# Optimization experiments

Hardware: AMD Instinct MI355X
Metric: run time of the kernel (lower is better)

Reference implementation:

```python
import jax, jax.numpy as jnp
import numpy as np

N = 100000
E = 1600000
F_IN = 32
H = 64
EDGE_DIM = 2
OUT = 1
NEG_SLOPE = 0.2


def setup_inputs() -> dict:
    key = jax.random.key(0)
    ks = jax.random.split(key, 20)
    g = lambda k, shape, fan_in: jax.random.normal(k, shape, jnp.float32) / np.sqrt(fan_in)
    inp = {
        "x": jax.random.normal(ks[0], (N, F_IN), jnp.float32),
        "edge_index": jax.random.randint(ks[1], (2, E), 0, N, jnp.int32),
        "edge_attr": jax.random.normal(ks[2], (E, EDGE_DIM), jnp.float32),
        # GATConv layer 1 (in=F_IN, out=H, heads=1, edge_dim=EDGE_DIM)
        "W1": g(ks[3], (F_IN, H), F_IN),
        "as1": g(ks[4], (H,), H),
        "ad1": g(ks[5], (H,), H),
        "We1": g(ks[6], (EDGE_DIM, H), EDGE_DIM),
        "ae1": g(ks[7], (H,), H),
        "b1": jnp.zeros((H,), jnp.float32),
        # GATConv layer 2 (in=H, out=H)
        "W2": g(ks[8], (H, H), H),
        "as2": g(ks[9], (H,), H),
        "ad2": g(ks[10], (H,), H),
        "We2": g(ks[11], (EDGE_DIM, H), EDGE_DIM),
        "ae2": g(ks[12], (H,), H),
        "b2": jnp.zeros((H,), jnp.float32),
        # Linear head
        "Wl": g(ks[13], (H, OUT), H),
        "bl": jnp.zeros((OUT,), jnp.float32),
    }
    return inp


def gat_conv(x, src, dst, edge_attr, W, att_src, att_dst, We, att_e, bias):
    """PyG GATConv, heads=1, add_self_loops=True (fill_value='mean'), eval mode."""
    n = x.shape[0]
    # add self-loops; self-loop edge_attr = mean of edge_attr (fill_value='mean')
    loop_attr = jnp.mean(edge_attr, axis=0)
    src_a = jnp.concatenate([src, jnp.arange(n, dtype=src.dtype)])
    dst_a = jnp.concatenate([dst, jnp.arange(n, dtype=dst.dtype)])
    ea = jnp.concatenate([edge_attr, jnp.broadcast_to(loop_attr, (n, edge_attr.shape[1]))])
    h = x @ W                          # [n, H]
    a_src = h @ att_src                # [n]
    a_dst = h @ att_dst                # [n]
    a_edge = (ea @ We) @ att_e         # [E+n]
    alpha = a_src[src_a] + a_dst[dst_a] + a_edge
    alpha = jax.nn.leaky_relu(alpha, NEG_SLOPE)
    # segment softmax over incoming edges of each destination node
    amax = jax.ops.segment_max(alpha, dst_a, num_segments=n)
    ex = jnp.exp(alpha - amax[dst_a])
    denom = jax.ops.segment_sum(ex, dst_a, num_segments=n)
    w = ex / denom[dst_a]              # every node has a self-loop -> denom > 0
    out = jax.ops.segment_sum(h[src_a] * w[:, None], dst_a, num_segments=n)
    return out + bias


def reference(x, edge_index, edge_attr, W1, as1, ad1, We1, ae1, b1,
              W2, as2, ad2, We2, ae2, b2, Wl, bl):
    src, dst = edge_index[0], edge_index[1]
    h = gat_conv(x, src, dst, edge_attr, W1, as1, ad1, We1, ae1, b1)
    h = jax.nn.relu(h)  # dropout is identity in eval mode
    h = gat_conv(h, src, dst, edge_attr, W2, as2, ad2, We2, ae2, b2)
    h = h @ Wl + bl
    return jax.nn.relu(h)
```

## Files before the change

### kernel.cpp

```cpp
#include <hip/hip_runtime.h>
#include <hip/hip_fp16.h>
#include <cstdint>

#define HH 64
#define NEG 0.2f
#define NB 256
#define SH 7
#define BKCAP 1024
#define ECAP 4096
#define CHCAP 6272

__device__ __forceinline__ float leaky(float x){ return x > 0.f ? x : NEG * x; }

__global__ void k_hist(const int* __restrict__ dst, const float* __restrict__ ea,
                       int* __restrict__ ghist, float2* __restrict__ pbuf,
                       int E, int nbkt, int CH){
    __shared__ int hist[BKCAP];
    __shared__ float2 sm[8];
    for (int i = threadIdx.x; i < nbkt; i += 512) hist[i] = 0;
    __syncthreads();
    int b = blockIdx.x;
    int e0 = b * CH, e1 = min(E, e0 + CH);
    float s0 = 0.f, s1 = 0.f;
    for (int e = e0 + threadIdx.x; e < e1; e += 512){
        int d = dst[e];
        atomicAdd(&hist[d >> SH], 1);
        float2 v = *reinterpret_cast<const float2*>(ea + 2ll * e);
        s0 += v.x; s1 += v.y;
    }
    #pragma unroll
    for (int o = 32; o; o >>= 1){ s0 += __shfl_xor(s0, o); s1 += __shfl_xor(s1, o); }
    int wv = threadIdx.x >> 6;
    if ((threadIdx.x & 63) == 0) sm[wv] = make_float2(s0, s1);
    __syncthreads();
    if (threadIdx.x == 0){
        float m0 = 0.f, m1 = 0.f;
        #pragma unroll
        for (int i = 0; i < 8; ++i){ m0 += sm[i].x; m1 += sm[i].y; }
        pbuf[b] = make_float2(m0, m1);
    }
    for (int i = threadIdx.x; i < nbkt; i += 512)
        ghist[(size_t)b * nbkt + i] = hist[i];
}

__global__ void k_const(const float* __restrict__ We1, const float* __restrict__ ae1,
                        const float* __restrict__ We2, const float* __restrict__ ae2,
                        const float2* __restrict__ pbuf, float* __restrict__ cbuf,
                        float invE, int nbp){
    int k = threadIdx.x;
    float m0 = 0.f, m1 = 0.f;
    for (int i = k; i < nbp; i += 64){ float2 u = pbuf[i]; m0 += u.x; m1 += u.y; }
    float p0 = We1[k] * ae1[k], p1 = We1[64 + k] * ae1[k];
    float q0 = We2[k] * ae2[k], q1 = We2[64 + k] * ae2[k];
    #pragma unroll
    for (int o = 32; o; o >>= 1){
        m0 += __shfl_xor(m0, o); m1 += __shfl_xor(m1, o);
        p0 += __shfl_xor(p0, o); p1 += __shfl_xor(p1, o);
        q0 += __shfl_xor(q0, o); q1 += __shfl_xor(q1, o);
    }
    if (k == 0){
        m0 *= invE; m1 *= invE;
        cbuf[4] = p0; cbuf[5] = p1; cbuf[6] = q0; cbuf[7] = q1;
        cbuf[2] = m0 * p0 + m1 * p1;
        cbuf[3] = m0 * q0 + m1 * q1;
    }
}

__global__ void k_scanA(const int* __restrict__ ghist, int* __restrict__ incl,
                        int* __restrict__ part, int M, int nbkt){
    __shared__ int sm[256];
    int tid = threadIdx.x;
    int i = blockIdx.x * 256 + tid;
    int v = 0;
    if (i < M) v = ghist[(size_t)(i % NB) * nbkt + (i / NB)];
    int x = v;
    sm[tid] = x; __syncthreads();
    for (int o = 1; o < 256; o <<= 1){
        int t = (tid >= o) ? sm[tid - o] : 0;
        __syncthreads();
        x += t; sm[tid] = x;
        __syncthreads();
    }
    if (i < M) incl[i] = x;
    if (tid == 255) part[blockIdx.x] = x;
}

__global__ void k_scanB(int* __restrict__ part, int nb){
    __shared__ int sm[1024];
    int tid = threadIdx.x;
    int C = (nb + 1023) >> 10;
    if (C > 8) C = 8;
    int base = tid * C;
    int vals[8];
    int s = 0;
    #pragma unroll
    for (int k = 0; k < 8; ++k){
        if (k < C){
            int i = base + k;
            int v = (i < nb) ? part[i] : 0;
            vals[k] = v; s += v;
        }
    }
    sm[tid] = s; __syncthreads();
    int x = s;
    for (int o = 1; o < 1024; o <<= 1){
        int t = (tid >= o) ? sm[tid - o] : 0;
        __syncthreads();
        x += t; sm[tid] = x;
        __syncthreads();
    }
    int excl = x - s;
    #pragma unroll
    for (int k = 0; k < 8; ++k){
        if (k < C){
            int i = base + k;
            if (i < nb){ int v = vals[k]; part[i] = excl; excl += v; }
        }
    }
}

__global__ void k_scanC(const int* __restrict__ ghist, const int* __restrict__ incl,
                        const int* __restrict__ part, int* __restrict__ gbase,
                        int M, int nbkt){
    int i = blockIdx.x * 256 + threadIdx.x;
    if (i < M){
        int v = ghist[(size_t)(i % NB) * nbkt + (i / NB)];
        gbase[i] = part[blockIdx.x] + incl[i] - v;
    }
}

__global__ void k_scatter2(const int* __restrict__ src, const int* __restrict__ dst,
                           const float* __restrict__ ea, const int* __restrict__ ghist,
                           const int* __restrict__ gbase, const float* __restrict__ cbuf,
                           uint2* __restrict__ csort, int E, int nbkt, int CH){
    __shared__ uint2 srec[CHCAP];
    __shared__ unsigned short bktof[CHCAP];
    __shared__ int gb[BKCAP];
    __shared__ int cur[BKCAP];
    __shared__ int wsum[512];
    int tid = threadIdx.x;
    int b = blockIdx.x;
    int base2 = tid * 2;
    int v0 = 0, v1 = 0;
    if (base2 < nbkt)     v0 = ghist[(size_t)b * nbkt + base2];
    if (base2 + 1 < nbkt) v1 = ghist[(size_t)b * nbkt + base2 + 1];
    int s = v0 + v1;
    wsum[tid] = s; __syncthreads();
    int x = s;
    for (int o = 1; o < 512; o <<= 1){
        int t = (tid >= o) ? wsum[tid - o] : 0;
        __syncthreads();
        x += t; wsum[tid] = x;
        __syncthreads();
    }
    int excl = x - s;
    if (base2 < nbkt)     cur[base2]     = excl;
    if (base2 + 1 < nbkt) cur[base2 + 1] = excl + v0;
    __syncthreads();
    for (int i = tid; i < nbkt; i += 512)
        gb[i] = gbase[(size_t)i * NB + b] - cur[i];
    __syncthreads();
    float c4 = cbuf[4], c5 = cbuf[5], c6 = cbuf[6], c7 = cbuf[7];
    int e0 = b * CH, e1 = min(E, e0 + CH);
    for (int e = e0 + tid; e < e1; e += 512){
        int d = dst[e];
        int bkt = d >> SH;
        float2 v = *reinterpret_cast<const float2*>(ea + 2ll * e);
        float a1 = v.x * c4 + v.y * c5;
        float a2 = v.x * c6 + v.y * c7;
        __half2 ah = __floats2half2_rn(a1, a2);
        int p = atomicAdd(&cur[bkt], 1);
        uint2 o;
        o.x = (unsigned)src[e] | ((unsigned)(d & ((1 << SH) - 1)) << 20);
        o.y = *reinterpret_cast<unsigned*>(&ah);
        srec[p] = o;
        bktof[p] = (unsigned short)bkt;
    }
    __syncthreads();
    int cnt = e1 - e0;
    for (int j = tid; j < cnt; j += 512)
        csort[gb[bktof[j]] + j] = srec[j];
}

__global__ void __launch_bounds__(256, 1) k_bucket(
        const uint2* __restrict__ csort, const int* __restrict__ gbase,
        uint2* __restrict__ rec, int* __restrict__ row_ptr,
        int E, int n, int nbkt){
    __shared__ uint2 lrec[ECAP];
    __shared__ uint2 srec[ECAP];
    __shared__ int nhist[128], ncur[128], sscan[128];
    int tid = threadIdx.x;
    int bkt = blockIdx.x;
    int base = gbase[(size_t)bkt * NB];
    int end  = (bkt + 1 < nbkt) ? gbase[(size_t)(bkt + 1) * NB] : E;
    int cnt = min(end - base, ECAP);
    if (tid < 128) nhist[tid] = 0;
    __syncthreads();
    for (int j = tid; j < cnt; j += 256){
        uint2 r = csort[base + j];
        lrec[j] = r;
        atomicAdd(&nhist[(r.x >> 20) & 127], 1);
    }
    __syncthreads();
    int v = (tid < 128) ? nhist[tid] : 0;
    if (tid < 128) sscan[tid] = v;
    __syncthreads();
    for (int o = 1; o < 128; o <<= 1){
        int t = 0;
        if (tid < 128 && tid >= o) t = sscan[tid - o];
        __syncthreads();
        if (tid < 128) sscan[tid] += t;
        __syncthreads();
    }
    if (tid < 128){
        int st = sscan[tid] - v;
        ncur[tid] = st;
        int node = (bkt << SH) + tid;
        if (node < n) row_ptr[node] = base + st;
    }
    if (bkt == 0 && tid == 255) row_ptr[n] = E;
    __syncthreads();
    for (int j = tid; j < cnt; j += 256){
        uint2 r = lrec[j];
        int dl = (r.x >> 20) & 127;
        int p = atomicAdd(&ncur[dl], 1);
        srec[p] = make_uint2(r.x & 0xFFFFFu, r.y);
    }
    __syncthreads();
    for (int j = tid; j < cnt; j += 256)
        rec[base + j] = srec[j];
}

template<int F, bool HALFIN>
__global__ void k_feat(const void* __restrict__ inp, const float* __restrict__ W,
                       const float* __restrict__ as_, const float* __restrict__ ad_,
                       __half* __restrict__ h, float* __restrict__ asrc,
                       float* __restrict__ adst, int n){
    int lane = threadIdx.x & 63;
    int wid0 = (blockIdx.x * blockDim.x + threadIdx.x) >> 6;
    int nw   = (gridDim.x * blockDim.x) >> 6;
    float wcol[F];
    #pragma unroll
    for (int i = 0; i < F; ++i) wcol[i] = W[i * HH + lane];
    float asl = as_[lane], adl = ad_[lane];
    for (int wid = wid0; wid < n; wid += nw){
        int u = __builtin_amdgcn_readfirstlane(wid);
        float a0 = 0.f, a1 = 0.f, a2 = 0.f, a3 = 0.f;
        if constexpr (!HALFIN){
            const float* __restrict__ row = (const float*)inp + (size_t)u * F;
            #pragma unroll
            for (int i = 0; i < F; i += 4){
                a0 += row[i]     * wcol[i];
                a1 += row[i + 1] * wcol[i + 1];
                a2 += row[i + 2] * wcol[i + 2];
                a3 += row[i + 3] * wcol[i + 3];
            }
        } else {
            const unsigned* __restrict__ row =
                (const unsigned*)((const __half*)inp + (size_t)u * F);
            #pragma unroll
            for (int i = 0; i < F / 2; i += 2){
                unsigned p0 = row[i], p1 = row[i + 1];
                __half2 h0 = *reinterpret_cast<__half2*>(&p0);
                __half2 h1 = *reinterpret_cast<__half2*>(&p1);
                float2 f0 = __half22float2(h0), f1 = __half22float2(h1);
                a0 += f0.x * wcol[2 * i];
                a1 += f0.y * wcol[2 * i + 1];
                a2 += f1.x * wcol[2 * i + 2];
                a3 += f1.y * wcol[2 * i + 3];
            }
        }
        float acc = (a0 + a1) + (a2 + a3);
        h[(size_t)u * HH + lane] = __float2half(acc);
        float vs = acc * asl, vd = acc * adl;
        #pragma unroll
        for (int o = 32; o; o >>= 1){ vs += __shfl_xor(vs, o); vd += __shfl_xor(vd, o); }
        if (lane == 0){ asrc[u] = vs; adst[u] = vd; }
    }
}

template<int AFIELD, bool RELU, bool HEAD>
__global__ void k_fused(const __half* __restrict__ h, const uint2* __restrict__ rec,
                        const int* __restrict__ row_ptr, const float* __restrict__ asrc,
                        const float* __restrict__ adst, const float* __restrict__ cbuf,
                        const float* __restrict__ bias, const float* __restrict__ Wl,
                        const float* __restrict__ bl, __half* __restrict__ outh,
                        float* __restrict__ outf, int n){
    int tid  = blockIdx.x * blockDim.x + threadIdx.x;
    int wave = tid >> 6;
    int lane = threadIdx.x & 63;
    int grp  = lane >> 3;
    int l7   = lane & 7;
    int node = wave * 8 + grp;
    bool valid = node < n;
    int nc = valid ? node : 0;
    int b  = row_ptr[nc];
    int e2 = valid ? row_ptr[nc + 1] : b;
    float ad = adst[nc];
    float aself = leaky(asrc[nc] + ad + cbuf[AFIELD == 1 ? 2 : 3]);
    float exs = __expf(aself);
    float dsum = exs;
    float acc[8];
    {
        float4 q = *reinterpret_cast<const float4*>(h + (size_t)nc * HH + (l7 << 3));
        const __half2* ph = reinterpret_cast<const __half2*>(&q);
        #pragma unroll
        for (int i = 0; i < 4; ++i){
            float2 f = __half22float2(ph[i]);
            acc[2 * i]     = exs * f.x;
            acc[2 * i + 1] = exs * f.y;
        }
    }
    auto pick = [](uint2 rr) -> float {
        __half2 ah = *reinterpret_cast<const __half2*>(&rr.y);
        return (AFIELD == 1) ? __low2float(ah) : __high2float(ah);
    };
    int j = b;
    for (; j + 3 < e2; j += 4){
        uint2 r0 = rec[j], r1 = rec[j + 1], r2 = rec[j + 2], r3 = rec[j + 3];
        int s0 = (int)r0.x, s1 = (int)r1.x, s2 = (int)r2.x, s3 = (int)r3.x;
        float w0 = __expf(leaky(asrc[s0] + ad + pick(r0)));
        float w1 = __expf(leaky(asrc[s1] + ad + pick(r1)));
        float w2 = __expf(leaky(asrc[s2] + ad + pick(r2)));
        float w3 = __expf(leaky(asrc[s3] + ad + pick(r3)));
        dsum += (w0 + w1) + (w2 + w3);
        float4 q0 = *reinterpret_cast<const float4*>(h + (size_t)s0 * HH + (l7 << 3));
        float4 q1 = *reinterpret_cast<const float4*>(h + (size_t)s1 * HH + (l7 << 3));
        float4 q2 = *reinterpret_cast<const float4*>(h + (size_t)s2 * HH + (l7 << 3));
        float4 q3 = *reinterpret_cast<const float4*>(h + (size_t)s3 * HH + (l7 << 3));
        const __half2* p0 = reinterpret_cast<const __half2*>(&q0);
        const __half2* p1 = reinterpret_cast<const __half2*>(&q1);
        const __half2* p2 = reinterpret_cast<const __half2*>(&q2);
        const __half2* p3 = reinterpret_cast<const __half2*>(&q3);
        #pragma unroll
        for (int i = 0; i < 4; ++i){
            float2 f0 = __half22float2(p0[i]);
            float2 f1 = __half22float2(p1[i]);
            float2 f2 = __half22float2(p2[i]);
            float2 f3 = __half22float2(p3[i]);
            acc[2 * i]     += w0 * f0.x + w1 * f1.x + w2 * f2.x + w3 * f3.x;
            acc[2 * i + 1] += w0 * f0.y + w1 * f1.y + w2 * f2.y + w3 * f3.y;
        }
    }
    for (; j < e2; ++j){
        uint2 rr = rec[j];
        int s = (int)rr.x;
        float w = __expf(leaky(asrc[s] + ad + pick(rr)));
        dsum += w;
        float4 q = *reinterpret_cast<const float4*>(h + (size_t)s * HH + (l7 << 3));
        const __half2* ph = reinterpret_cast<const __half2*>(&q);
        #pragma unroll
        for (int i = 0; i < 4; ++i){
            float2 f = __half22float2(ph[i]);
            acc[2 * i]     += w * f.x;
            acc[2 * i + 1] += w * f.y;
        }
    }
    float inv = 1.f / dsum;
    float4 b0 = *reinterpret_cast<const float4*>(bias + (l7 << 3));
    float4 b1 = *reinterpret_cast<const float4*>(bias + (l7 << 3) + 4);
    float r[8];
    r[0] = acc[0] * inv + b0.x; r[1] = acc[1] * inv + b0.y;
    r[2] = acc[2] * inv + b0.z; r[3] = acc[3] * inv + b0.w;
    r[4] = acc[4] * inv + b1.x; r[5] = acc[5] * inv + b1.y;
    r[6] = acc[6] * inv + b1.z; r[7] = acc[7] * inv + b1.w;
    if (RELU){
        #pragma unroll
        for (int i = 0; i < 8; ++i) r[i] = fmaxf(r[i], 0.f);
    }
    if (!HEAD){
        if (valid){
            __half2 q01 = __floats2half2_rn(r[0], r[1]);
            __half2 q23 = __floats2half2_rn(r[2], r[3]);
            __half2 q45 = __floats2half2_rn(r[4], r[5]);
            __half2 q67 = __floats2half2_rn(r[6], r[7]);
            uint4 st;
            st.x = *reinterpret_cast<unsigned*>(&q01);
            st.y = *reinterpret_cast<unsigned*>(&q23);
            st.z = *reinterpret_cast<unsigned*>(&q45);
            st.w = *reinterpret_cast<unsigned*>(&q67);
            *reinterpret_cast<uint4*>(outh + (size_t)node * HH + (l7 << 3)) = st;
        }
    } else {
        float4 w0 = *reinterpret_cast<const float4*>(Wl + (l7 << 3));
        float4 w1 = *reinterpret_cast<const float4*>(Wl + (l7 << 3) + 4);
        float v = r[0] * w0.x + r[1] * w0.y + r[2] * w0.z + r[3] * w0.w
                + r[4] * w1.x + r[5] * w1.y + r[6] * w1.z + r[7] * w1.w;
        v += __shfl_xor(v, 1); v += __shfl_xor(v, 2); v += __shfl_xor(v, 4);
        if (valid && l7 == 0) outf[node] = fmaxf(v + bl[0], 0.f);
    }
}

extern "C" void kernel_launch(void* const* d_in, const int* in_sizes, int n_in,
                              void* d_out, int out_size, void* d_ws, size_t ws_size,
                              hipStream_t stream) {
    const float* x   = (const float*)d_in[0];
    const int*   ei  = (const int*)  d_in[1];
    const float* ea  = (const float*)d_in[2];
    const float* W1  = (const float*)d_in[3];
    const float* as1 = (const float*)d_in[4];
    const float* ad1 = (const float*)d_in[5];
    const float* We1 = (const float*)d_in[6];
    const float* ae1 = (const float*)d_in[7];
    const float* b1  = (const float*)d_in[8];
    const float* W2  = (const float*)d_in[9];
    const float* as2 = (const float*)d_in[10];
    const float* ad2 = (const float*)d_in[11];
    const float* We2 = (const float*)d_in[12];
    const float* ae2 = (const float*)d_in[13];
    const float* b2  = (const float*)d_in[14];
    const float* Wl  = (const float*)d_in[15];
    const float* bl  = (const float*)d_in[16];
    float* out = (float*)d_out;

    const int N = in_sizes[0] / 32;
    const int E = in_sizes[1] / 2;
    const int* srcI = ei;
    const int* dstI = ei + E;

    const int nbkt = (N + (1 << SH) - 1) >> SH;
    const int M    = nbkt * NB;
    const int CH   = (E + NB - 1) / NB;
    const int gMs  = (M + 255) / 256;

    char* ws = (char*)d_ws;
    size_t off = 0;
    auto alloc = [&](size_t bytes)->char*{
        char* p = ws + off;
        off += (bytes + 255) & ~size_t(255);
        return p;
    };
    __half*  hbuf   = (__half*) alloc((size_t)N * HH * 2);
    __half*  bufB   = (__half*) alloc((size_t)N * HH * 2);
    uint2*   rec    = (uint2*)  alloc((size_t)E * 8);
    uint2*   csort  = (uint2*)  alloc((size_t)E * 8);
    int*     ghist  = (int*)    alloc((size_t)M * 4);
    int*     incl   = (int*)    alloc((size_t)M * 4);
    int*     gbase  = (int*)    alloc((size_t)M * 4);
    int*     part   = (int*)    alloc((size_t)gMs * 4);
    int*     row_ptr= (int*)    alloc((size_t)(N + 1) * 4);
    float*   asrc   = (float*)  alloc((size_t)N * 4);
    float*   adst   = (float*)  alloc((size_t)N * 4);
    float2*  pbuf   = (float2*) alloc((size_t)NB * 8);
    float*   cbuf   = (float*)  alloc(64);
    if (off > ws_size) return;

    const int BLK = 256;
    int gF = ((size_t)N * 8 + BLK - 1) / BLK;

    k_hist<<<NB, 512, 0, stream>>>(dstI, ea, ghist, pbuf, E, nbkt, CH);
    k_const<<<1, 64, 0, stream>>>(We1, ae1, We2, ae2, pbuf, cbuf, 1.f / (float)E, NB);
    k_scanA<<<gMs, 256, 0, stream>>>(ghist, incl, part, M, nbkt);
    k_scanB<<<1, 1024, 0, stream>>>(part, gMs);
    k_scanC<<<gMs, 256, 0, stream>>>(ghist, incl, part, gbase, M, nbkt);
    k_scatter2<<<NB, 512, 0, stream>>>(srcI, dstI, ea, ghist, gbase, cbuf, csort, E, nbkt, CH);
    k_bucket<<<nbkt, BLK, 0, stream>>>(csort, gbase, rec, row_ptr, E, N, nbkt);

    k_feat<32, false><<<2048, BLK, 0, stream>>>(x, W1, as1, ad1, hbuf, asrc, adst, N);
    k_fused<1, true, false><<<gF, BLK, 0, stream>>>(hbuf, rec, row_ptr, asrc, adst,
                                                    cbuf, b1, nullptr, nullptr, bufB, nullptr, N);

    k_feat<64, true><<<2048, BLK, 0, stream>>>(bufB, W2, as2, ad2, hbuf, asrc, adst, N);
    k_fused<2, false, true><<<gF, BLK, 0, stream>>>(hbuf, rec, row_ptr, asrc, adst,
                                                    cbuf, b2, Wl, bl, nullptr, out, N);
}
```

Before: 177.8 us.

## Fuse per-bucket CSR sort into aggregation kernels, drop k_bucket pass

Removes the separate bucket-sorting kernel that wrote a global CSR record array and row pointers. Each aggregation kernel now loads its bucket's edge records from csort, sorts them by local destination in shared memory, and then aggregates 128 nodes per block with 32 groups of 8 lanes, four rounds each. This saves one launch and the global write and reread of the sorted records. In exchange the local sort is repeated in both layers, and the aggregation now runs with only 782 blocks, each holding 32KB of shared memory, which may reduce occupancy and latency hiding for the gathers.

Result: no change. 175.4 us (-1.4%).

```diff
diff --git a/kernel.cpp b/kernel.cpp
--- a/kernel.cpp
+++ b/kernel.cpp
@@ -182,55 +182,6 @@
         csort[gb[bktof[j]] + j] = srec[j];
 }
 
-__global__ void __launch_bounds__(256, 1) k_bucket(
-        const uint2* __restrict__ csort, const int* __restrict__ gbase,
-        uint2* __restrict__ rec, int* __restrict__ row_ptr,
-        int E, int n, int nbkt){
-    __shared__ uint2 lrec[ECAP];
-    __shared__ uint2 srec[ECAP];
-    __shared__ int nhist[128], ncur[128], sscan[128];
-    int tid = threadIdx.x;
-    int bkt = blockIdx.x;
-    int base = gbase[(size_t)bkt * NB];
-    int end  = (bkt + 1 < nbkt) ? gbase[(size_t)(bkt + 1) * NB] : E;
-    int cnt = min(end - base, ECAP);
-    if (tid < 128) nhist[tid] = 0;
-    __syncthreads();
-    for (int j = tid; j < cnt; j += 256){
-        uint2 r = csort[base + j];
-        lrec[j] = r;
-        atomicAdd(&nhist[(r.x >> 20) & 127], 1);
-    }
-    __syncthreads();
-    int v = (tid < 128) ? nhist[tid] : 0;
-    if (tid < 128) sscan[tid] = v;
-    __syncthreads();
-    for (int o = 1; o < 128; o <<= 1){
-        int t = 0;
-        if (tid < 128 && tid >= o) t = sscan[tid - o];
-        __syncthreads();
-        if (tid < 128) sscan[tid] += t;
-        __syncthreads();
-    }
-    if (tid < 128){
-        int st = sscan[tid] - v;
-        ncur[tid] = st;
-        int node = (bkt << SH) + tid;
-        if (node < n) row_ptr[node] = base + st;
-    }
-    if (bkt == 0 && tid == 255) row_ptr[n] = E;
-    __syncthreads();
-    for (int j = tid; j < cnt; j += 256){
-        uint2 r = lrec[j];
-        int dl = (r.x >> 20) & 127;
-        int p = atomicAdd(&ncur[dl], 1);
-        srec[p] = make_uint2(r.x & 0xFFFFFu, r.y);
-    }
-    __syncthreads();
-    for (int j = tid; j < cnt; j += 256)
-        rec[base + j] = srec[j];
-}
-
 template<int F, bool HALFIN>
 __global__ void k_feat(const void* __restrict__ inp, const float* __restrict__ W,
                        const float* __restrict__ as_, const float* __restrict__ ad_,
@@ -280,96 +231,129 @@
 }
 
 template<int AFIELD, bool RELU, bool HEAD>
-__global__ void k_fused(const __half* __restrict__ h, const uint2* __restrict__ rec,
-                        const int* __restrict__ row_ptr, const float* __restrict__ asrc,
-                        const float* __restrict__ adst, const float* __restrict__ cbuf,
-                        const float* __restrict__ bias, const float* __restrict__ Wl,
-                        const float* __restrict__ bl, __half* __restrict__ outh,
-                        float* __restrict__ outf, int n){
-    int tid  = blockIdx.x * blockDim.x + threadIdx.x;
-    int wave = tid >> 6;
-    int lane = threadIdx.x & 63;
-    int grp  = lane >> 3;
-    int l7   = lane & 7;
-    int node = wave * 8 + grp;
-    bool valid = node < n;
-    int nc = valid ? node : 0;
-    int b  = row_ptr[nc];
-    int e2 = valid ? row_ptr[nc + 1] : b;
-    float ad = adst[nc];
-    float aself = leaky(asrc[nc] + ad + cbuf[AFIELD == 1 ? 2 : 3]);
-    float exs = __expf(aself);
-    float dsum = exs;
-    float acc[8];
-    {
-        float4 q = *reinterpret_cast<const float4*>(h + (size_t)nc * HH + (l7 << 3));
-        const __half2* ph = reinterpret_cast<const __half2*>(&q);
-        #pragma unroll
-        for (int i = 0; i < 4; ++i){
-            float2 f = __half22float2(ph[i]);
-            acc[2 * i]     = exs * f.x;
-            acc[2 * i + 1] = exs * f.y;
-        }
-    }
+__global__ void __launch_bounds__(256) k_fused4(
+        const __half* __restrict__ h, const uint2* __restrict__ csort,
+        const int* __restrict__ gbase, const float* __restrict__ asrc,
+        const float* __restrict__ adst, const float* __restrict__ cbuf,
+        const float* __restrict__ bias, const float* __restrict__ Wl,
+        const float* __restrict__ bl, __half* __restrict__ outh,
+        float* __restrict__ outf, int E, int n, int nbkt){
+    __shared__ uint2 srec[ECAP];
+    __shared__ int nhist[128], sscan[128], ncur[128];
+    int tid = threadIdx.x, bkt = blockIdx.x;
+    int base = gbase[(size_t)bkt * NB];
+    int end  = (bkt + 1 < nbkt) ? gbase[(size_t)(bkt + 1) * NB] : E;
+    int cnt  = min(end - base, ECAP);
+    int node0 = bkt << SH;
+    if (tid < 128) nhist[tid] = 0;
+    __syncthreads();
+    for (int j = tid; j < cnt; j += 256){
+        uint2 r = csort[base + j];
+        atomicAdd(&nhist[(r.x >> 20) & 127], 1);
+    }
+    __syncthreads();
+    int v = (tid < 128) ? nhist[tid] : 0;
+    if (tid < 128) sscan[tid] = v;
+    __syncthreads();
+    for (int o = 1; o < 128; o <<= 1){
+        int t = 0;
+        if (tid < 128 && tid >= o) t = sscan[tid - o];
+        __syncthreads();
+        if (tid < 128) sscan[tid] += t;
+        __syncthreads();
+    }
+    if (tid < 128) ncur[tid] = sscan[tid] - v;
+    __syncthreads();
+    for (int j = tid; j < cnt; j += 256){
+        uint2 r = csort[base + j];
+        int p = atomicAdd(&ncur[(r.x >> 20) & 127], 1);
+        srec[p] = r;
+    }
+    __syncthreads();
+
+    int g = tid >> 3, l7 = tid & 7;
+    float cself = cbuf[AFIELD == 1 ? 2 : 3];
     auto pick = [](uint2 rr) -> float {
         __half2 ah = *reinterpret_cast<const __half2*>(&rr.y);
         return (AFIELD == 1) ? __low2float(ah) : __high2float(ah);
     };
-    int j = b;
-    for (; j + 3 < e2; j += 4){
-        uint2 r0 = rec[j], r1 = rec[j + 1], r2 = rec[j + 2], r3 = rec[j + 3];
-        int s0 = (int)r0.x, s1 = (int)r1.x, s2 = (int)r2.x, s3 = (int)r3.x;
-        float w0 = __expf(leaky(asrc[s0] + ad + pick(r0)));
-        float w1 = __expf(leaky(asrc[s1] + ad + pick(r1)));
-        float w2 = __expf(leaky(asrc[s2] + ad + pick(r2)));
-        float w3 = __expf(leaky(asrc[s3] + ad + pick(r3)));
-        dsum += (w0 + w1) + (w2 + w3);
-        float4 q0 = *reinterpret_cast<const float4*>(h + (size_t)s0 * HH + (l7 << 3));
-        float4 q1 = *reinterpret_cast<const float4*>(h + (size_t)s1 * HH + (l7 << 3));
-        float4 q2 = *reinterpret_cast<const float4*>(h + (size_t)s2 * HH + (l7 << 3));
-        float4 q3 = *reinterpret_cast<const float4*>(h + (size_t)s3 * HH + (l7 << 3));
-        const __half2* p0 = reinterpret_cast<const __half2*>(&q0);
-        const __half2* p1 = reinterpret_cast<const __half2*>(&q1);
-        const __half2* p2 = reinterpret_cast<const __half2*>(&q2);
-        const __half2* p3 = reinterpret_cast<const __half2*>(&q3);
-        #pragma unroll
-        for (int i = 0; i < 4; ++i){
-            float2 f0 = __half22float2(p0[i]);
-            float2 f1 = __half22float2(p1[i]);
-            float2 f2 = __half22float2(p2[i]);
-            float2 f3 = __half22float2(p3[i]);
-            acc[2 * i]     += w0 * f0.x + w1 * f1.x + w2 * f2.x + w3 * f3.x;
-            acc[2 * i + 1] += w0 * f0.y + w1 * f1.y + w2 * f2.y + w3 * f3.y;
-        }
-    }
-    for (; j < e2; ++j){
-        uint2 rr = rec[j];
-        int s = (int)rr.x;
-        float w = __expf(leaky(asrc[s] + ad + pick(rr)));
-        dsum += w;
-        float4 q = *reinterpret_cast<const float4*>(h + (size_t)s * HH + (l7 << 3));
-        const __half2* ph = reinterpret_cast<const __half2*>(&q);
-        #pragma unroll
-        for (int i = 0; i < 4; ++i){
-            float2 f = __half22float2(ph[i]);
-            acc[2 * i]     += w * f.x;
-            acc[2 * i + 1] += w * f.y;
-        }
-    }
-    float inv = 1.f / dsum;
-    float4 b0 = *reinterpret_cast<const float4*>(bias + (l7 << 3));
-    float4 b1 = *reinterpret_cast<const float4*>(bias + (l7 << 3) + 4);
-    float r[8];
-    r[0] = acc[0] * inv + b0.x; r[1] = acc[1] * inv + b0.y;
-    r[2] = acc[2] * inv + b0.z; r[3] = acc[3] * inv + b0.w;
-    r[4] = acc[4] * inv + b1.x; r[5] = acc[5] * inv + b1.y;
-    r[6] = acc[6] * inv + b1.z; r[7] = acc[7] * inv + b1.w;
-    if (RELU){
-        #pragma unroll
-        for (int i = 0; i < 8; ++i) r[i] = fmaxf(r[i], 0.f);
-    }
-    if (!HEAD){
-        if (valid){
+    #pragma unroll
+    for (int rd = 0; rd < 4; ++rd){
+        int nl = g + rd * 32;
+        int node = node0 + nl;
+        if (node >= n) continue;
+        int ke = sscan[nl];
+        int kb = ke - nhist[nl];
+        float ad = adst[node];
+        float aself = leaky(asrc[node] + ad + cself);
+        float exs = __expf(aself);
+        float dsum = exs;
+        float acc[8];
+        {
+            float4 q = *reinterpret_cast<const float4*>(h + (size_t)node * HH + (l7 << 3));
+            const __half2* ph = reinterpret_cast<const __half2*>(&q);
+            #pragma unroll
+            for (int i = 0; i < 4; ++i){
+                float2 f = __half22float2(ph[i]);
+                acc[2 * i]     = exs * f.x;
+                acc[2 * i + 1] = exs * f.y;
+            }
+        }
+        int k = kb;
+        for (; k + 3 < ke; k += 4){
+            uint2 r0 = srec[k], r1 = srec[k + 1], r2 = srec[k + 2], r3 = srec[k + 3];
+            int s0 = r0.x & 0xFFFFF, s1 = r1.x & 0xFFFFF;
+            int s2 = r2.x & 0xFFFFF, s3 = r3.x & 0xFFFFF;
+            float w0 = __expf(leaky(asrc[s0] + ad + pick(r0)));
+            float w1 = __expf(leaky(asrc[s1] + ad + pick(r1)));
+            float w2 = __expf(leaky(asrc[s2] + ad + pick(r2)));
+            float w3 = __expf(leaky(asrc[s3] + ad + pick(r3)));
+            dsum += (w0 + w1) + (w2 + w3);
+            float4 q0 = *reinterpret_cast<const float4*>(h + (size_t)s0 * HH + (l7 << 3));
+            float4 q1 = *reinterpret_cast<const float4*>(h + (size_t)s1 * HH + (l7 << 3));
+            float4 q2 = *reinterpret_cast<const float4*>(h + (size_t)s2 * HH + (l7 << 3));
+            float4 q3 = *reinterpret_cast<const float4*>(h + (size_t)s3 * HH + (l7 << 3));
+            const __half2* p0 = reinterpret_cast<const __half2*>(&q0);
+            const __half2* p1 = reinterpret_cast<const __half2*>(&q1);
+            const __half2* p2 = reinterpret_cast<const __half2*>(&q2);
+            const __half2* p3 = reinterpret_cast<const __half2*>(&q3);
+            #pragma unroll
+            for (int i = 0; i < 4; ++i){
+                float2 f0 = __half22float2(p0[i]);
+                float2 f1 = __half22float2(p1[i]);
+                float2 f2 = __half22float2(p2[i]);
+                float2 f3 = __half22float2(p3[i]);
+                acc[2 * i]     += w0 * f0.x + w1 * f1.x + w2 * f2.x + w3 * f3.x;
+                acc[2 * i + 1] += w0 * f0.y + w1 * f1.y + w2 * f2.y + w3 * f3.y;
+            }
+        }
+        for (; k < ke; ++k){
+            uint2 rr = srec[k];
+            int s = rr.x & 0xFFFFF;
+            float w = __expf(leaky(asrc[s] + ad + pick(rr)));
+            dsum += w;
+            float4 q = *reinterpret_cast<const float4*>(h + (size_t)s * HH + (l7 << 3));
+            const __half2* ph = reinterpret_cast<const __half2*>(&q);
+            #pragma unroll
+            for (int i = 0; i < 4; ++i){
+                float2 f = __half22float2(ph[i]);
+                acc[2 * i]     += w * f.x;
+                acc[2 * i + 1] += w * f.y;
+            }
+        }
+        float inv = 1.f / dsum;
+        float4 b0 = *reinterpret_cast<const float4*>(bias + (l7 << 3));
+        float4 b1 = *reinterpret_cast<const float4*>(bias + (l7 << 3) + 4);
+        float r[8];
+        r[0] = acc[0] * inv + b0.x; r[1] = acc[1] * inv + b0.y;
+        r[2] = acc[2] * inv + b0.z; r[3] = acc[3] * inv + b0.w;
+        r[4] = acc[4] * inv + b1.x; r[5] = acc[5] * inv + b1.y;
+        r[6] = acc[6] * inv + b1.z; r[7] = acc[7] * inv + b1.w;
+        if (RELU){
+            #pragma unroll
+            for (int i = 0; i < 8; ++i) r[i] = fmaxf(r[i], 0.f);
+        }
+        if (!HEAD){
             __half2 q01 = __floats2half2_rn(r[0], r[1]);
             __half2 q23 = __floats2half2_rn(r[2], r[3]);
             __half2 q45 = __floats2half2_rn(r[4], r[5]);
@@ -380,14 +364,14 @@
             st.z = *reinterpret_cast<unsigned*>(&q45);
             st.w = *reinterpret_cast<unsigned*>(&q67);
             *reinterpret_cast<uint4*>(outh + (size_t)node * HH + (l7 << 3)) = st;
-        }
-    } else {
-        float4 w0 = *reinterpret_cast<const float4*>(Wl + (l7 << 3));
-        float4 w1 = *reinterpret_cast<const float4*>(Wl + (l7 << 3) + 4);
-        float v = r[0] * w0.x + r[1] * w0.y + r[2] * w0.z + r[3] * w0.w
-                + r[4] * w1.x + r[5] * w1.y + r[6] * w1.z + r[7] * w1.w;
-        v += __shfl_xor(v, 1); v += __shfl_xor(v, 2); v += __shfl_xor(v, 4);
-        if (valid && l7 == 0) outf[node] = fmaxf(v + bl[0], 0.f);
+        } else {
+            float4 w0 = *reinterpret_cast<const float4*>(Wl + (l7 << 3));
+            float4 w1 = *reinterpret_cast<const float4*>(Wl + (l7 << 3) + 4);
+            float vv = r[0] * w0.x + r[1] * w0.y + r[2] * w0.z + r[3] * w0.w
+                     + r[4] * w1.x + r[5] * w1.y + r[6] * w1.z + r[7] * w1.w;
+            vv += __shfl_xor(vv, 1); vv += __shfl_xor(vv, 2); vv += __shfl_xor(vv, 4);
+            if (l7 == 0) outf[node] = fmaxf(vv + bl[0], 0.f);
+        }
     }
 }
 
@@ -432,13 +416,11 @@
     };
     __half*  hbuf   = (__half*) alloc((size_t)N * HH * 2);
     __half*  bufB   = (__half*) alloc((size_t)N * HH * 2);
-    uint2*   rec    = (uint2*)  alloc((size_t)E * 8);
     uint2*   csort  = (uint2*)  alloc((size_t)E * 8);
     int*     ghist  = (int*)    alloc((size_t)M * 4);
     int*     incl   = (int*)    alloc((size_t)M * 4);
     int*     gbase  = (int*)    alloc((size_t)M * 4);
     int*     part   = (int*)    alloc((size_t)gMs * 4);
-    int*     row_ptr= (int*)    alloc((size_t)(N + 1) * 4);
     float*   asrc   = (float*)  alloc((size_t)N * 4);
     float*   adst   = (float*)  alloc((size_t)N * 4);
     float2*  pbuf   = (float2*) alloc((size_t)NB * 8);
@@ -446,7 +428,6 @@
     if (off > ws_size) return;
 
     const int BLK = 256;
-    int gF = ((size_t)N * 8 + BLK - 1) / BLK;
 
     k_hist<<<NB, 512, 0, stream>>>(dstI, ea, ghist, pbuf, E, nbkt, CH);
     k_const<<<1, 64, 0, stream>>>(We1, ae1, We2, ae2, pbuf, cbuf, 1.f / (float)E, NB);
@@ -454,13 +435,14 @@
     k_scanB<<<1, 1024, 0, stream>>>(part, gMs);
     k_scanC<<<gMs, 256, 0, stream>>>(ghist, incl, part, gbase, M, nbkt);
     k_scatter2<<<NB, 512, 0, stream>>>(srcI, dstI, ea, ghist, gbase, cbuf, csort, E, nbkt, CH);
-    k_bucket<<<nbkt, BLK, 0, stream>>>(csort, gbase, rec, row_ptr, E, N, nbkt);
 
     k_feat<32, false><<<2048, BLK, 0, stream>>>(x, W1, as1, ad1, hbuf, asrc, adst, N);
-    k_fused<1, true, false><<<gF, BLK, 0, stream>>>(hbuf, rec, row_ptr, asrc, adst,
-                                                    cbuf, b1, nullptr, nullptr, bufB, nullptr, N);
+    k_fused4<1, true, false><<<nbkt, BLK, 0, stream>>>(hbuf, csort, gbase, asrc, adst,
+                                                       cbuf, b1, nullptr, nullptr,
+                                                       bufB, nullptr, E, N, nbkt);
 
     k_feat<64, true><<<2048, BLK, 0, stream>>>(bufB, W2, as2, ad2, hbuf, asrc, adst, N);
-    k_fused<2, false, true><<<gF, BLK, 0, stream>>>(hbuf, rec, row_ptr, asrc, adst,
-                                                    cbuf, b2, Wl, bl, nullptr, out, N);
-}
+    k_fused4<2, false, true><<<nbkt, BLK, 0, stream>>>(hbuf, csort, gbase, asrc, adst,
+                                                       cbuf, b2, Wl, bl,
+                                                       nullptr, out, E, N, nbkt);
+}
```
